# Kernel optimization log

Measured on AMD Instinct MI355X. Metric: run time of the kernel, lower is better.

The kernel has to match this reference:

```python
import jax, jax.numpy as jnp
import numpy as np

NUM_CLASSES = 10
MAX_V = 81  # max_width * max_height = 9*9


def _ln(x, w, eps=1e-5):
    # torch LayerNorm with bias=False (weight only)
    m = jnp.mean(x, axis=-1, keepdims=True)
    v = jnp.var(x, axis=-1, keepdims=True)
    return (x - m) / jnp.sqrt(v + eps) * w


def _mha(q_in, k_in, v_in, in_proj, out_proj, nhead):
    # torch nn.MultiheadAttention, bias=False
    d = q_in.shape[-1]
    Wq, Wk, Wv = in_proj[:d], in_proj[d:2 * d], in_proj[2 * d:]
    q = q_in @ Wq.T
    k = k_in @ Wk.T
    v = v_in @ Wv.T
    B, Lq, _ = q.shape
    Lk = k.shape[1]
    hd = d // nhead
    q = q.reshape(B, Lq, nhead, hd)
    k = k.reshape(B, Lk, nhead, hd)
    v = v.reshape(B, Lk, nhead, hd)
    scores = jnp.einsum('bqhd,bkhd->bhqk', q, k) / jnp.sqrt(jnp.asarray(hd, q.dtype))
    attn = jax.nn.softmax(scores, axis=-1)
    o = jnp.einsum('bhqk,bkhd->bqhd', attn, v).reshape(B, Lq, d)
    return o @ out_proj.T


def setup_inputs() -> dict:
    key = jax.random.key(0)
    ks = jax.random.split(key, 16)
    N, C, H, W = 16, NUM_CLASSES, 30, 30
    d = C + 1  # 11
    V = 32

    def rn(k, shape, s=0.2):
        return (jax.random.normal(k, shape) * s).astype(jnp.float32)

    return {
        'x': jax.random.normal(ks[0], (N, C, H, W), dtype=jnp.float32),
        'V_feature': rn(ks[1], (C, V), 1.0),
        'enc_in_proj': rn(ks[2], (3 * d, d)),
        'enc_out_proj': rn(ks[3], (d, d)),
        'enc_lin1': rn(ks[4], (1, d)),
        'enc_lin2': rn(ks[5], (d, 1)),
        'enc_ln1': jnp.ones((d,), jnp.float32),
        'enc_ln2': jnp.ones((d,), jnp.float32),
        'ffV_w': rn(ks[6], (V, MAX_V)),
        'dec_sa_in': rn(ks[7], (3 * V, V)),
        'dec_sa_out': rn(ks[8], (V, V)),
        'dec_ca_in': rn(ks[9], (3 * V, V)),
        'dec_ca_out': rn(ks[10], (V, V)),
        'dec_lin1': rn(ks[11], (1, V)),
        'dec_lin2': rn(ks[12], (V, 1)),
        'dec_ln1': jnp.ones((V,), jnp.float32),
        'dec_ln2': jnp.ones((V,), jnp.float32),
        'dec_ln3': jnp.ones((V,), jnp.float32),
        'W_d0': rn(ks[13], (8, V)),
        'W_d1': rn(ks[14], (1, 8)),
    }


def reference(x, V_feature, enc_in_proj, enc_out_proj, enc_lin1, enc_lin2,
              enc_ln1, enc_ln2, ffV_w, dec_sa_in, dec_sa_out, dec_ca_in,
              dec_ca_out, dec_lin1, dec_lin2, dec_ln1, dec_ln2, dec_ln3,
              W_d0, W_d1):
    N, C, H, W = x.shape
    # PixelVectorExtractor: pad(0) + all-ones channel padded with 1, 3x3 unfold
    xp = jnp.pad(x, ((0, 0), (0, 0), (1, 1), (1, 1)))
    ones = jnp.ones((N, 1, H + 2, W + 2), x.dtype)
    xc = jnp.concatenate([xp, ones], axis=1)  # [N, C+1, H+2, W+2]
    # row-major 3x3 patch order matches torch unfold(0,3,1).unfold(1,3,1)
    patches = jnp.stack([xc[:, :, di:di + H, dj:dj + W]
                         for di in range(3) for dj in range(3)], axis=-1)
    feat = patches.transpose(0, 2, 3, 1, 4).reshape(N * H * W, C + 1, 9)
    feat = jnp.pad(feat, ((0, 0), (0, 0), (0, MAX_V - 9)))  # [B, C+1, 81]

    # TransformerEncoder (1 layer, post-norm, nhead=1, relu FF, no dropout)
    f = feat.transpose(0, 2, 1)  # [B, 81, C+1]
    f = _ln(f + _mha(f, f, f, enc_in_proj, enc_out_proj, 1), enc_ln1)
    f = _ln(f + jax.nn.relu(f @ enc_lin1.T) @ enc_lin2.T, enc_ln2)
    f = f.transpose(0, 2, 1)  # [B, C+1, 81]

    mem = f @ ffV_w.T  # ff_V: Linear(81 -> 32, no bias) -> [B, C+1, 32]
    B, _, V = mem.shape

    # TransformerDecoder (1 layer, post-norm, nhead=32 so head_dim=1)
    y = jnp.broadcast_to(V_feature, (B, C, V))
    y = _ln(y + _mha(y, y, y, dec_sa_in, dec_sa_out, V), dec_ln1)
    y = _ln(y + _mha(y, mem, mem, dec_ca_in, dec_ca_out, V), dec_ln2)
    y = _ln(y + jax.nn.relu(y @ dec_lin1.T) @ dec_lin2.T, dec_ln3)

    # decode MLP: 32 -> 8 -> 1
    y = jax.nn.relu(y @ W_d0.T) @ W_d1.T  # [B, C, 1]
    return y.reshape(N, H, W, C).transpose(0, 3, 1, 2)
```

## Files before the change

kernel.cpp:

```cpp
#include <hip/hip_runtime.h>
#include <math.h>


__device__ __forceinline__ float gsum32(float v) {
#pragma unroll
  for (int m = 16; m > 0; m >>= 1) v += __shfl_xor(v, m, 32);
  return v;
}

__device__ __forceinline__ void wsync() {
  asm volatile("s_waitcnt lgkmcnt(0)" ::: "memory");
}

__global__ __launch_bounds__(256) void precompute_kernel(
    const float* __restrict__ Vf,
    const float* __restrict__ enc_in,
    const float* __restrict__ enc_outw,
    const float* __restrict__ ffV_w,
    const float* __restrict__ dec_sa_in,
    const float* __restrict__ dec_sa_out,
    const float* __restrict__ dec_ln1,
    const float* __restrict__ dec_ca_in,
    float* __restrict__ M_enc, float* __restrict__ WVO,
    float* __restrict__ G_k, float* __restrict__ G_v,
    float* __restrict__ y1, float* __restrict__ qca)
{
  const int tid = threadIdx.x;

  if (blockIdx.x == 0) {
    const float rs11 = 0.3015113445777636f;
    for (int idx = tid; idx < 121; idx += 256) {
      int c = idx / 11, cp = idx - c * 11;
      float sm = 0.f, sv = 0.f;
      for (int i = 0; i < 11; ++i) {
        sm += enc_in[i * 11 + c] * enc_in[(11 + i) * 11 + cp];
        sv += enc_outw[c * 11 + i] * enc_in[(22 + i) * 11 + cp];
      }
      M_enc[idx] = sm * rs11;
      WVO[idx] = sv;
    }

    __shared__ float Fsh[320];
    for (int idx = tid; idx < 288; idx += 256) {
      int t = idx >> 5, j = idx & 31;
      Fsh[idx] = ffV_w[j * 81 + t];
    }
    if (tid < 32) {
      float s = 0.f;
      for (int t = 9; t < 81; ++t) s += ffV_w[tid * 81 + t];
      Fsh[288 + tid] = s;
    }
    __syncthreads();

    for (int idx = tid; idx < 640; idx += 256) {
      int which = idx >= 320;
      int r = idx - 320 * which;
      int t = r >> 5, h = r & 31;
      const float* w = dec_ca_in + ((which ? 64 : 32) + h) * 32;
      float s = 0.f;
      for (int j = 0; j < 32; ++j) s += Fsh[t * 32 + j] * w[j];
      (which ? G_v : G_k)[r] = s;
    }
  } else {
    __shared__ float qsa[320], ksa[320], vsa[320], osa[320], zb[320];
    __shared__ float mu[16], rstd[16];

    for (int idx = tid; idx < 960; idx += 256) {
      int m = idx / 320, r = idx - m * 320;
      int t = r >> 5, h = r & 31;
      const float* w = dec_sa_in + (m * 32 + h) * 32;
      const float* yr = Vf + t * 32;
      float s = 0.f;
#pragma unroll
      for (int j = 0; j < 32; ++j) s += yr[j] * w[j];
      (m == 0 ? qsa : m == 1 ? ksa : vsa)[r] = s;
    }
    __syncthreads();

    for (int idx = tid; idx < 320; idx += 256) {
      int h = idx & 31;
      float q = qsa[idx];
      float sc[10];
      float mx = -1e30f;
#pragma unroll
      for (int s = 0; s < 10; ++s) { sc[s] = q * ksa[s * 32 + h]; mx = fmaxf(mx, sc[s]); }
      float den = 0.f, acc = 0.f;
#pragma unroll
      for (int s = 0; s < 10; ++s) {
        float e = __expf(sc[s] - mx);
        den += e;
        acc += e * vsa[s * 32 + h];
      }
      osa[idx] = acc / den;
    }
    __syncthreads();

    for (int idx = tid; idx < 320; idx += 256) {
      int t = idx >> 5, c = idx & 31;
      float s = 0.f;
#pragma unroll
      for (int h = 0; h < 32; ++h) s += osa[t * 32 + h] * dec_sa_out[c * 32 + h];
      zb[idx] = Vf[idx] + s;
    }
    __syncthreads();

    if (tid < 10) {
      float s1 = 0.f, s2 = 0.f;
      for (int c = 0; c < 32; ++c) { float z = zb[tid * 32 + c]; s1 += z; s2 += z * z; }
      float m = s1 * (1.f / 32.f);
      mu[tid] = m;
      rstd[tid] = 1.f / sqrtf(s2 * (1.f / 32.f) - m * m + 1e-5f);
    }
    __syncthreads();

    for (int idx = tid; idx < 320; idx += 256) {
      int t = idx >> 5, c = idx & 31;
      float v = (zb[idx] - mu[t]) * rstd[t] * dec_ln1[c];
      y1[idx] = v;
      zb[idx] = v;
    }
    __syncthreads();

    for (int idx = tid; idx < 320; idx += 256) {
      int t = idx >> 5, h = idx & 31;
      const float* w = dec_ca_in + h * 32;
      float s = 0.f;
#pragma unroll
      for (int j = 0; j < 32; ++j) s += zb[t * 32 + j] * w[j];
      qca[idx] = s;
    }
  }
}

#define SLICE 1376

__global__ __launch_bounds__(256) void pixel_main_kernel(
    const float* __restrict__ x,
    const float* __restrict__ M_enc, const float* __restrict__ WVO,
    const float* __restrict__ enc_lin1, const float* __restrict__ enc_lin2,
    const float* __restrict__ enc_ln1, const float* __restrict__ enc_ln2,
    const float* __restrict__ G_k, const float* __restrict__ G_v,
    const float* __restrict__ y1g, const float* __restrict__ qcag,
    const float* __restrict__ dec_ca_out,
    const float* __restrict__ dec_lin1, const float* __restrict__ dec_lin2,
    const float* __restrict__ dec_ln2v, const float* __restrict__ dec_ln3v,
    const float* __restrict__ W_d0, const float* __restrict__ W_d1,
    float* __restrict__ out)
{
  __shared__ __align__(16) float sh[4 * SLICE];
  const int wave = threadIdx.x >> 6;
  const int lane = threadIdx.x & 63;
  float* ls = sh + wave * SLICE;
  const int F9 = 0, G = 112, VO = 224, SC = 336, ZR = 432, FE = 544, KC = 656, VC = 1008;
  const int OC = 0, ZB = 320;

  const int p = blockIdx.x * 4 + wave;
  const int n = p / 900;
  const int rem = p - n * 900;
  const int pi = rem / 30, pj = rem - (rem / 30) * 30;

  for (int idx = lane; idx < 99; idx += 64) {
    int t = idx / 11, c = idx - t * 11;
    float val = 1.0f;
    if (c < 10) {
      int di = t / 3, dj = t - (t / 3) * 3;
      int ii = pi + di - 1, jj = pj + dj - 1;
      val = (ii >= 0 && ii < 30 && jj >= 0 && jj < 30)
                ? x[((n * 10 + c) * 30 + ii) * 30 + jj] : 0.0f;
    }
    ls[F9 + idx] = val;
  }
  wsync();

  for (int idx = lane; idx < 99; idx += 64) {
    int s = idx / 11, c = idx - (idx / 11) * 11;
    const float* Mr = M_enc + c * 11;
    const float* Wr = WVO + c * 11;
    float ag = 0.f, av = 0.f;
#pragma unroll
    for (int cp = 0; cp < 11; ++cp) {
      float fv = ls[F9 + s * 11 + cp];
      ag += Mr[cp] * fv;
      av += Wr[cp] * fv;
    }
    ls[G + idx] = ag;
    ls[VO + idx] = av;
  }
  wsync();

  for (int idx = lane; idx < 81; idx += 64) {
    int t = idx / 9, s = idx - (idx / 9) * 9;
    float a = 0.f;
#pragma unroll
    for (int c = 0; c < 11; ++c) a += ls[F9 + t * 11 + c] * ls[G + s * 11 + c];
    ls[SC + idx] = a;
  }
  wsync();

  if (lane < 9) {
    float e[9];
    float mx = 0.0f;
#pragma unroll
    for (int s = 0; s < 9; ++s) { e[s] = ls[SC + lane * 9 + s]; mx = fmaxf(mx, e[s]); }
    float den = 72.0f * __expf(-mx);
#pragma unroll
    for (int s = 0; s < 9; ++s) {
      e[s] = __expf(e[s] - mx);
      den += e[s];
      ls[SC + lane * 9 + s] = e[s];
    }
    ls[SC + 81 + lane] = 1.0f / den;
  }
  wsync();

  for (int idx = lane; idx < 110; idx += 64) {
    int t = idx / 11, c = idx - (idx / 11) * 11;
    float a = 0.f;
    if (t < 9) {
#pragma unroll
      for (int s = 0; s < 9; ++s) a += ls[SC + t * 9 + s] * ls[VO + s * 11 + c];
      a = a * ls[SC + 81 + t] + ls[F9 + idx];
    } else {
#pragma unroll
      for (int s = 0; s < 9; ++s) a += ls[VO + s * 11 + c];
      a *= (1.0f / 81.0f);
    }
    ls[ZR + idx] = a;
  }
  wsync();

  if (lane < 10) {
    float row[11];
#pragma unroll
    for (int c = 0; c < 11; ++c) row[c] = ls[ZR + lane * 11 + c];
    float s1 = 0.f, s2 = 0.f;
#pragma unroll
    for (int c = 0; c < 11; ++c) { s1 += row[c]; s2 += row[c] * row[c]; }
    float mu = s1 * (1.0f / 11.0f);
    float rs = 1.0f / sqrtf(s2 * (1.0f / 11.0f) - mu * mu + 1e-5f);
    float h = 0.f;
#pragma unroll
    for (int c = 0; c < 11; ++c) {
      row[c] = (row[c] - mu) * rs * enc_ln1[c];
      h += row[c] * enc_lin1[c];
    }
    h = fmaxf(h, 0.f);
    float t1 = 0.f, t2 = 0.f;
#pragma unroll
    for (int c = 0; c < 11; ++c) {
      row[c] += h * enc_lin2[c];
      t1 += row[c]; t2 += row[c] * row[c];
    }
    float mu2 = t1 * (1.0f / 11.0f);
    float rs2 = 1.0f / sqrtf(t2 * (1.0f / 11.0f) - mu2 * mu2 + 1e-5f);
#pragma unroll
    for (int c = 0; c < 11; ++c)
      ls[FE + lane * 11 + c] = (row[c] - mu2) * rs2 * enc_ln2[c];
  }
  wsync();

  {
    const int h = lane & 31, grp = lane >> 5;
    const float* Gb = grp ? G_v : G_k;
    const int dst = grp ? VC : KC;
    float gr[10];
#pragma unroll
    for (int t = 0; t < 10; ++t) gr[t] = Gb[t * 32 + h];
#pragma unroll
    for (int c = 0; c < 11; ++c) {
      float a = 0.f;
#pragma unroll
      for (int t = 0; t < 10; ++t) a += ls[FE + t * 11 + c] * gr[t];
      ls[dst + c * 32 + h] = a;
    }
  }
  wsync();

  for (int it = 0; it < 5; ++it) {
    int idx = it * 64 + lane;
    int t = idx >> 5, h = idx & 31;
    float q = qcag[t * 32 + h];
    float kreg[11];
#pragma unroll
    for (int s = 0; s < 11; ++s) kreg[s] = q * ls[KC + s * 32 + h];
    float mx = kreg[0];
#pragma unroll
    for (int s = 1; s < 11; ++s) mx = fmaxf(mx, kreg[s]);
    float den = 0.f, acc = 0.f;
#pragma unroll
    for (int s = 0; s < 11; ++s) {
      float e = __expf(kreg[s] - mx);
      den += e;
      acc += e * ls[VC + s * 32 + h];
    }
    ls[OC + idx] = acc / den;
  }
  wsync();

  for (int k = 0; k < 5; ++k) {
    int t = 2 * k + (lane >> 5);
    int c = lane & 31;
    float zacc = 0.f;
    const float4* wrow = (const float4*)(dec_ca_out + c * 32);
    const float4* orow = (const float4*)(ls + OC + t * 32);
#pragma unroll
    for (int h4 = 0; h4 < 8; ++h4) {
      float4 o4 = orow[h4];
      float4 w4 = wrow[h4];
      zacc += o4.x * w4.x + o4.y * w4.y + o4.z * w4.z + o4.w * w4.w;
    }
    float z = y1g[t * 32 + c] + zacc;
    {
      float s1 = gsum32(z), s2 = gsum32(z * z);
      float mu = s1 * (1.0f / 32.0f);
      z = (z - mu) * (1.0f / sqrtf(s2 * (1.0f / 32.0f) - mu * mu + 1e-5f)) * dec_ln2v[c];
    }
    {
      float d1 = gsum32(z * dec_lin1[c]);
      z += fmaxf(d1, 0.f) * dec_lin2[c];
    }
    {
      float s1 = gsum32(z), s2 = gsum32(z * z);
      float mu = s1 * (1.0f / 32.0f);
      z = (z - mu) * (1.0f / sqrtf(s2 * (1.0f / 32.0f) - mu * mu + 1e-5f)) * dec_ln3v[c];
    }
    ls[ZB + t * 32 + c] = z;
  }
  wsync();

  for (int idx = lane; idx < 80; idx += 64) {
    int t = idx >> 3, m = idx & 7;
    const float4* arow = (const float4*)(W_d0 + m * 32);
    const float4* zrow4 = (const float4*)(ls + ZB + t * 32);
    float d = 0.f;
#pragma unroll
    for (int q4 = 0; q4 < 8; ++q4) {
      float4 a4 = arow[q4];
      float4 z4 = zrow4[q4];
      d += a4.x * z4.x + a4.y * z4.y + a4.z * z4.z + a4.w * z4.w;
    }
    ls[OC + idx] = fmaxf(d, 0.f);
  }
  wsync();

  if (lane < 10) {
    float r = 0.f;
#pragma unroll
    for (int m = 0; m < 8; ++m) r += ls[OC + lane * 8 + m] * W_d1[m];
    out[((n * 10 + lane) * 30 + pi) * 30 + pj] = r;
  }
}

extern "C" void kernel_launch(void* const* d_in, const int* in_sizes, int n_in,
                              void* d_out, int out_size, void* d_ws, size_t ws_size,
                              hipStream_t stream) {
  (void)in_sizes; (void)n_in; (void)out_size; (void)ws_size;
  const float* x          = (const float*)d_in[0];
  const float* Vf         = (const float*)d_in[1];
  const float* enc_in     = (const float*)d_in[2];
  const float* enc_outw   = (const float*)d_in[3];
  const float* enc_lin1   = (const float*)d_in[4];
  const float* enc_lin2   = (const float*)d_in[5];
  const float* enc_ln1    = (const float*)d_in[6];
  const float* enc_ln2    = (const float*)d_in[7];
  const float* ffV_w      = (const float*)d_in[8];
  const float* dec_sa_in  = (const float*)d_in[9];
  const float* dec_sa_out = (const float*)d_in[10];
  const float* dec_ca_in  = (const float*)d_in[11];
  const float* dec_ca_out = (const float*)d_in[12];
  const float* dec_lin1   = (const float*)d_in[13];
  const float* dec_lin2   = (const float*)d_in[14];
  const float* dec_ln1    = (const float*)d_in[15];
  const float* dec_ln2    = (const float*)d_in[16];
  const float* dec_ln3    = (const float*)d_in[17];
  const float* W_d0       = (const float*)d_in[18];
  const float* W_d1       = (const float*)d_in[19];
  float* out = (float*)d_out;

  float* ws    = (float*)d_ws;
  float* M_enc = ws;
  float* WVO   = ws + 128;
  float* G_k   = ws + 256;
  float* G_v   = ws + 576;
  float* y1    = ws + 896;
  float* qca   = ws + 1216;

  hipLaunchKernelGGL(precompute_kernel, dim3(2), dim3(256), 0, stream,
                     Vf, enc_in, enc_outw, ffV_w, dec_sa_in, dec_sa_out,
                     dec_ln1, dec_ca_in, M_enc, WVO, G_k, G_v, y1, qca);

  hipLaunchKernelGGL(pixel_main_kernel, dim3(3600), dim3(256), 0, stream,
                     x, M_enc, WVO, enc_lin1, enc_lin2, enc_ln1, enc_ln2,
                     G_k, G_v, y1, qca, dec_ca_out, dec_lin1, dec_lin2,
                     dec_ln2, dec_ln3, W_d0, W_d1, out);
}
```

Baseline: 171.5 us.

## Fold decoder LayerNorm/FFN/MLP tail algebraically and pad LDS layouts for vector loads

The pixel kernel's decoder tail changes. Instead of two LayerNorms, the FFN and the 32→8 MLP done with many shuffle reductions and LDS round-trips, each lane now computes 15 partial sums that are reduced with ds_swizzle. The final outputs come from constants precomputed in the setup kernel (hc). LDS arrays are padded to stride 12 so float4 loads work, the per-wave slice shrinks, and K/V for cross-attention are kept in registers and exchanged with a shuffle. Other changes: exp2 with LOG2E folded into the weights, rcp/rsq intrinsics, and encoder matrices staged in LDS. The algebraic expansion of the variance terms may lose some precision.

```diff
diff --git a/kernel.cpp b/kernel.cpp
--- a/kernel.cpp
+++ b/kernel.cpp
@@ -2,11 +2,18 @@
 #include <math.h>
 
 
-__device__ __forceinline__ float gsum32(float v) {
-#pragma unroll
-  for (int m = 16; m > 0; m >>= 1) v += __shfl_xor(v, m, 32);
-  return v;
-}
+#define LOG2E 1.4426950408889634f
+
+#define F9o   0
+#define Go    112
+#define VOTo  224
+#define SCo   368
+#define ZRo   512
+#define FETo  640
+#define OCo   0
+#define SLICE 784
+
+#define SWZ_ADD(v, pat) ((v) + __int_as_float(__builtin_amdgcn_ds_swizzle(__float_as_int(v), (pat))))
 
 __device__ __forceinline__ void wsync() {
   asm volatile("s_waitcnt lgkmcnt(0)" ::: "memory");
@@ -21,9 +28,12 @@
     const float* __restrict__ dec_sa_out,
     const float* __restrict__ dec_ln1,
     const float* __restrict__ dec_ca_in,
+    const float* __restrict__ dec_ln2v, const float* __restrict__ dec_lin1,
+    const float* __restrict__ dec_lin2, const float* __restrict__ dec_ln3v,
+    const float* __restrict__ W_d0,
     float* __restrict__ M_enc, float* __restrict__ WVO,
     float* __restrict__ G_k, float* __restrict__ G_v,
-    float* __restrict__ y1, float* __restrict__ qca)
+    float* __restrict__ y1, float* __restrict__ qca, float* __restrict__ hc)
 {
   const int tid = threadIdx.x;
 
@@ -36,7 +46,7 @@
         sm += enc_in[i * 11 + c] * enc_in[(11 + i) * 11 + cp];
         sv += enc_outw[c * 11 + i] * enc_in[(22 + i) * 11 + cp];
       }
-      M_enc[idx] = sm * rs11;
+      M_enc[idx] = sm * rs11 * LOG2E;
       WVO[idx] = sv;
     }
 
@@ -60,6 +70,25 @@
       float s = 0.f;
       for (int j = 0; j < 32; ++j) s += Fsh[t * 32 + j] * w[j];
       (which ? G_v : G_k)[r] = s;
+    }
+
+    if (tid < 8) {
+      float u = 0.f, t2 = 0.f, v = 0.f;
+      for (int c = 0; c < 32; ++c) {
+        float w0 = W_d0[tid * 32 + c] * dec_ln3v[c];
+        u += dec_ln2v[c] * w0;
+        t2 += dec_lin2[c] * w0;
+        v += w0;
+      }
+      hc[tid] = u; hc[8 + tid] = t2; hc[16 + tid] = v;
+    } else if (tid == 8) {
+      float a = 0, b = 0, c2 = 0, d = 0, e = 0, f = 0;
+      for (int c = 0; c < 32; ++c) {
+        float w2 = dec_ln2v[c], l2 = dec_lin2[c];
+        a += w2; b += w2 * dec_lin1[c]; c2 += w2 * w2;
+        d += w2 * l2; e += l2; f += l2 * l2;
+      }
+      hc[24] = a; hc[25] = b; hc[26] = c2; hc[27] = d; hc[28] = e; hc[29] = f;
     }
   } else {
     __shared__ float qsa[320], ksa[320], vsa[320], osa[320], zb[320];
@@ -127,12 +156,10 @@
       float s = 0.f;
 #pragma unroll
       for (int j = 0; j < 32; ++j) s += zb[t * 32 + j] * w[j];
-      qca[idx] = s;
+      qca[idx] = s * LOG2E;
     }
   }
 }
-
-#define SLICE 1376
 
 __global__ __launch_bounds__(256) void pixel_main_kernel(
     const float* __restrict__ x,
@@ -142,17 +169,23 @@
     const float* __restrict__ G_k, const float* __restrict__ G_v,
     const float* __restrict__ y1g, const float* __restrict__ qcag,
     const float* __restrict__ dec_ca_out,
-    const float* __restrict__ dec_lin1, const float* __restrict__ dec_lin2,
-    const float* __restrict__ dec_ln2v, const float* __restrict__ dec_ln3v,
+    const float* __restrict__ dec_ln2v, const float* __restrict__ dec_lin1,
+    const float* __restrict__ dec_lin2, const float* __restrict__ dec_ln3v,
     const float* __restrict__ W_d0, const float* __restrict__ W_d1,
+    const float* __restrict__ hc,
     float* __restrict__ out)
 {
-  __shared__ __align__(16) float sh[4 * SLICE];
+  __shared__ __align__(16) float sh[4 * SLICE + 256];
+  float* bc = sh + 4 * SLICE;
+  for (int i = threadIdx.x; i < 121; i += 256) {
+    bc[i] = M_enc[i];
+    bc[128 + i] = WVO[i];
+  }
+  __syncthreads();
+
   const int wave = threadIdx.x >> 6;
   const int lane = threadIdx.x & 63;
   float* ls = sh + wave * SLICE;
-  const int F9 = 0, G = 112, VO = 224, SC = 336, ZR = 432, FE = 544, KC = 656, VC = 1008;
-  const int OC = 0, ZB = 320;
 
   const int p = blockIdx.x * 4 + wave;
   const int n = p / 900;
@@ -168,76 +201,84 @@
       val = (ii >= 0 && ii < 30 && jj >= 0 && jj < 30)
                 ? x[((n * 10 + c) * 30 + ii) * 30 + jj] : 0.0f;
     }
-    ls[F9 + idx] = val;
-  }
+    ls[F9o + t * 12 + c] = val;
+  }
+  if (lane < 12) ls[SCo + 108 + lane] = (lane < 9) ? (1.0f / 81.0f) : 0.0f;
   wsync();
 
   for (int idx = lane; idx < 99; idx += 64) {
     int s = idx / 11, c = idx - (idx / 11) * 11;
-    const float* Mr = M_enc + c * 11;
-    const float* Wr = WVO + c * 11;
+    const float4* fr = (const float4*)(ls + F9o + s * 12);
+    float4 f0 = fr[0], f1 = fr[1], f2 = fr[2];
+    float fv[11] = {f0.x, f0.y, f0.z, f0.w, f1.x, f1.y, f1.z, f1.w, f2.x, f2.y, f2.z};
+    const float* Mr = bc + c * 11;
+    const float* Wr = bc + 128 + c * 11;
     float ag = 0.f, av = 0.f;
 #pragma unroll
-    for (int cp = 0; cp < 11; ++cp) {
-      float fv = ls[F9 + s * 11 + cp];
-      ag += Mr[cp] * fv;
-      av += Wr[cp] * fv;
-    }
-    ls[G + idx] = ag;
-    ls[VO + idx] = av;
+    for (int cp = 0; cp < 11; ++cp) { ag += Mr[cp] * fv[cp]; av += Wr[cp] * fv[cp]; }
+    ls[Go + s * 12 + c] = ag;
+    ls[VOTo + c * 12 + s] = av;
   }
   wsync();
 
   for (int idx = lane; idx < 81; idx += 64) {
     int t = idx / 9, s = idx - (idx / 9) * 9;
-    float a = 0.f;
-#pragma unroll
-    for (int c = 0; c < 11; ++c) a += ls[F9 + t * 11 + c] * ls[G + s * 11 + c];
-    ls[SC + idx] = a;
+    const float4* fr = (const float4*)(ls + F9o + t * 12);
+    const float4* gr = (const float4*)(ls + Go + s * 12);
+    float4 f0 = fr[0], f1 = fr[1], f2 = fr[2];
+    float4 g0 = gr[0], g1 = gr[1], g2 = gr[2];
+    float a = f0.x * g0.x + f0.y * g0.y + f0.z * g0.z + f0.w * g0.w
+            + f1.x * g1.x + f1.y * g1.y + f1.z * g1.z + f1.w * g1.w
+            + f2.x * g2.x + f2.y * g2.y + f2.z * g2.z;
+    ls[SCo + t * 12 + s] = a;
   }
   wsync();
 
   if (lane < 9) {
-    float e[9];
+    const float4* sr = (const float4*)(ls + SCo + lane * 12);
+    float4 s0 = sr[0], s1 = sr[1];
+    float sc[9] = {s0.x, s0.y, s0.z, s0.w, s1.x, s1.y, s1.z, s1.w,
+                   ls[SCo + lane * 12 + 8]};
     float mx = 0.0f;
 #pragma unroll
-    for (int s = 0; s < 9; ++s) { e[s] = ls[SC + lane * 9 + s]; mx = fmaxf(mx, e[s]); }
-    float den = 72.0f * __expf(-mx);
-#pragma unroll
-    for (int s = 0; s < 9; ++s) {
-      e[s] = __expf(e[s] - mx);
-      den += e[s];
-      ls[SC + lane * 9 + s] = e[s];
-    }
-    ls[SC + 81 + lane] = 1.0f / den;
+    for (int s = 0; s < 9; ++s) mx = fmaxf(mx, sc[s]);
+    float den = 72.0f * exp2f(-mx);
+    float e[12];
+    e[9] = e[10] = e[11] = 0.f;
+#pragma unroll
+    for (int s = 0; s < 9; ++s) { e[s] = exp2f(sc[s] - mx); den += e[s]; }
+    float4* dst = (float4*)(ls + SCo + lane * 12);
+    dst[0] = make_float4(e[0], e[1], e[2], e[3]);
+    dst[1] = make_float4(e[4], e[5], e[6], e[7]);
+    dst[2] = make_float4(e[8], 0.f, 0.f, 0.f);
+    ls[SCo + 120 + lane] = __builtin_amdgcn_rcpf(den);
   }
   wsync();
 
   for (int idx = lane; idx < 110; idx += 64) {
     int t = idx / 11, c = idx - (idx / 11) * 11;
-    float a = 0.f;
-    if (t < 9) {
-#pragma unroll
-      for (int s = 0; s < 9; ++s) a += ls[SC + t * 9 + s] * ls[VO + s * 11 + c];
-      a = a * ls[SC + 81 + t] + ls[F9 + idx];
-    } else {
-#pragma unroll
-      for (int s = 0; s < 9; ++s) a += ls[VO + s * 11 + c];
-      a *= (1.0f / 81.0f);
-    }
-    ls[ZR + idx] = a;
+    const float4* wr = (const float4*)(ls + SCo + t * 12);
+    const float4* vr = (const float4*)(ls + VOTo + c * 12);
+    float4 w0 = wr[0], w1 = wr[1], w2q = wr[2];
+    float4 v0 = vr[0], v1 = vr[1], v2 = vr[2];
+    float a = w0.x * v0.x + w0.y * v0.y + w0.z * v0.z + w0.w * v0.w
+            + w1.x * v1.x + w1.y * v1.y + w1.z * v1.z + w1.w * v1.w
+            + w2q.x * v2.x;
+    if (t < 9) a = a * ls[SCo + 120 + t] + ls[F9o + t * 12 + c];
+    ls[ZRo + t * 12 + c] = a;
   }
   wsync();
 
   if (lane < 10) {
-    float row[11];
-#pragma unroll
-    for (int c = 0; c < 11; ++c) row[c] = ls[ZR + lane * 11 + c];
+    const float4* zr = (const float4*)(ls + ZRo + lane * 12);
+    float4 z0 = zr[0], z1 = zr[1], z2q = zr[2];
+    float row[11] = {z0.x, z0.y, z0.z, z0.w, z1.x, z1.y, z1.z, z1.w,
+                     z2q.x, z2q.y, z2q.z};
     float s1 = 0.f, s2 = 0.f;
 #pragma unroll
     for (int c = 0; c < 11; ++c) { s1 += row[c]; s2 += row[c] * row[c]; }
     float mu = s1 * (1.0f / 11.0f);
-    float rs = 1.0f / sqrtf(s2 * (1.0f / 11.0f) - mu * mu + 1e-5f);
+    float rs = __builtin_amdgcn_rsqf(s2 * (1.0f / 11.0f) - mu * mu + 1e-5f);
     float h = 0.f;
 #pragma unroll
     for (int c = 0; c < 11; ++c) {
@@ -252,102 +293,118 @@
       t1 += row[c]; t2 += row[c] * row[c];
     }
     float mu2 = t1 * (1.0f / 11.0f);
-    float rs2 = 1.0f / sqrtf(t2 * (1.0f / 11.0f) - mu2 * mu2 + 1e-5f);
+    float rs2 = __builtin_amdgcn_rsqf(t2 * (1.0f / 11.0f) - mu2 * mu2 + 1e-5f);
 #pragma unroll
     for (int c = 0; c < 11; ++c)
-      ls[FE + lane * 11 + c] = (row[c] - mu2) * rs2 * enc_ln2[c];
-  }
-  wsync();
-
+      ls[FETo + c * 12 + lane] = (row[c] - mu2) * rs2 * enc_ln2[c];
+  }
+  wsync();
+
+  const int hh = lane & 31, grp = lane >> 5;
+  float kv[11];
   {
-    const int h = lane & 31, grp = lane >> 5;
     const float* Gb = grp ? G_v : G_k;
-    const int dst = grp ? VC : KC;
     float gr[10];
 #pragma unroll
-    for (int t = 0; t < 10; ++t) gr[t] = Gb[t * 32 + h];
-#pragma unroll
-    for (int c = 0; c < 11; ++c) {
-      float a = 0.f;
-#pragma unroll
-      for (int t = 0; t < 10; ++t) a += ls[FE + t * 11 + c] * gr[t];
-      ls[dst + c * 32 + h] = a;
-    }
-  }
-  wsync();
-
-  for (int it = 0; it < 5; ++it) {
-    int idx = it * 64 + lane;
-    int t = idx >> 5, h = idx & 31;
-    float q = qcag[t * 32 + h];
-    float kreg[11];
-#pragma unroll
-    for (int s = 0; s < 11; ++s) kreg[s] = q * ls[KC + s * 32 + h];
-    float mx = kreg[0];
-#pragma unroll
-    for (int s = 1; s < 11; ++s) mx = fmaxf(mx, kreg[s]);
+    for (int t = 0; t < 10; ++t) gr[t] = Gb[t * 32 + hh];
+#pragma unroll
+    for (int cc = 0; cc < 11; ++cc) {
+      const float4* fr = (const float4*)(ls + FETo + cc * 12);
+      float4 a = fr[0], b4 = fr[1], c4 = fr[2];
+      float fe[10] = {a.x, a.y, a.z, a.w, b4.x, b4.y, b4.z, b4.w, c4.x, c4.y};
+      float s = 0.f;
+#pragma unroll
+      for (int t = 0; t < 10; ++t) s += fe[t] * gr[t];
+      kv[cc] = s;
+    }
+  }
+  float kk[11], vv[11];
+#pragma unroll
+  for (int cc = 0; cc < 11; ++cc) {
+    float o = __shfl_xor(kv[cc], 32);
+    kk[cc] = grp ? o : kv[cc];
+    vv[cc] = grp ? kv[cc] : o;
+  }
+
+#pragma unroll
+  for (int i = 0; i < 5; ++i) {
+    int t = grp * 5 + i;
+    float q = qcag[t * 32 + hh];
+    float sc[11];
+    float mx = q * kk[0];
+    sc[0] = mx;
+#pragma unroll
+    for (int s = 1; s < 11; ++s) { sc[s] = q * kk[s]; mx = fmaxf(mx, sc[s]); }
     float den = 0.f, acc = 0.f;
 #pragma unroll
     for (int s = 0; s < 11; ++s) {
-      float e = __expf(kreg[s] - mx);
+      float e = exp2f(sc[s] - mx);
       den += e;
-      acc += e * ls[VC + s * 32 + h];
-    }
-    ls[OC + idx] = acc / den;
-  }
-  wsync();
-
+      acc += e * vv[s];
+    }
+    ls[OCo + t * 32 + hh] = acc * __builtin_amdgcn_rcpf(den);
+  }
+  wsync();
+
+  const int c = hh;
+  float w2 = dec_ln2v[c], cl1 = dec_lin1[c], cl2 = dec_lin2[c], w3 = dec_ln3v[c];
+  float cw2l1 = w2 * cl1, cw2sq = w2 * w2, cw2l2 = w2 * cl2;
+  float am[8], Uu[8], Tt[8], Vv[8], W1r[8];
+#pragma unroll
+  for (int m = 0; m < 8; ++m) {
+    am[m] = w2 * w3 * W_d0[m * 32 + c];
+    Uu[m] = hc[m]; Tt[m] = hc[8 + m]; Vv[m] = hc[16 + m]; W1r[m] = W_d1[m];
+  }
+  const float Sw2 = hc[24], Sw2l1 = hc[25], Sw2sq = hc[26], Sw2l2 = hc[27],
+              Sl2 = hc[28], Sl2sq = hc[29];
+  const float4* wrow = (const float4*)(dec_ca_out + c * 32);
+
+#pragma unroll
   for (int k = 0; k < 5; ++k) {
-    int t = 2 * k + (lane >> 5);
-    int c = lane & 31;
-    float zacc = 0.f;
-    const float4* wrow = (const float4*)(dec_ca_out + c * 32);
-    const float4* orow = (const float4*)(ls + OC + t * 32);
+    const int t = 2 * k + grp;
+    float z = y1g[t * 32 + c];
+    const float4* orow = (const float4*)(ls + OCo + t * 32);
 #pragma unroll
     for (int h4 = 0; h4 < 8; ++h4) {
       float4 o4 = orow[h4];
       float4 w4 = wrow[h4];
-      zacc += o4.x * w4.x + o4.y * w4.y + o4.z * w4.z + o4.w * w4.w;
-    }
-    float z = y1g[t * 32 + c] + zacc;
-    {
-      float s1 = gsum32(z), s2 = gsum32(z * z);
-      float mu = s1 * (1.0f / 32.0f);
-      z = (z - mu) * (1.0f / sqrtf(s2 * (1.0f / 32.0f) - mu * mu + 1e-5f)) * dec_ln2v[c];
-    }
-    {
-      float d1 = gsum32(z * dec_lin1[c]);
-      z += fmaxf(d1, 0.f) * dec_lin2[c];
-    }
-    {
-      float s1 = gsum32(z), s2 = gsum32(z * z);
-      float mu = s1 * (1.0f / 32.0f);
-      z = (z - mu) * (1.0f / sqrtf(s2 * (1.0f / 32.0f) - mu * mu + 1e-5f)) * dec_ln3v[c];
-    }
-    ls[ZB + t * 32 + c] = z;
-  }
-  wsync();
-
-  for (int idx = lane; idx < 80; idx += 64) {
-    int t = idx >> 3, m = idx & 7;
-    const float4* arow = (const float4*)(W_d0 + m * 32);
-    const float4* zrow4 = (const float4*)(ls + ZB + t * 32);
-    float d = 0.f;
-#pragma unroll
-    for (int q4 = 0; q4 < 8; ++q4) {
-      float4 a4 = arow[q4];
-      float4 z4 = zrow4[q4];
-      d += a4.x * z4.x + a4.y * z4.y + a4.z * z4.z + a4.w * z4.w;
-    }
-    ls[OC + idx] = fmaxf(d, 0.f);
-  }
-  wsync();
-
-  if (lane < 10) {
+      z += o4.x * w4.x + o4.y * w4.y + o4.z * w4.z + o4.w * w4.w;
+    }
+    float b[15];
+    b[0] = z; b[1] = z * z; b[2] = z * w2; b[3] = z * cw2l1;
+    b[4] = z * cw2sq; b[5] = b[1] * cw2sq; b[6] = z * cw2l2;
+#pragma unroll
+    for (int m = 0; m < 8; ++m) b[7 + m] = z * am[m];
+#pragma unroll
+    for (int i_ = 0; i_ < 15; ++i_) b[i_] = SWZ_ADD(b[i_], 0x041F);
+#pragma unroll
+    for (int i_ = 0; i_ < 15; ++i_) b[i_] = SWZ_ADD(b[i_], 0x081F);
+#pragma unroll
+    for (int i_ = 0; i_ < 15; ++i_) b[i_] = SWZ_ADD(b[i_], 0x101F);
+#pragma unroll
+    for (int i_ = 0; i_ < 15; ++i_) b[i_] = SWZ_ADD(b[i_], 0x201F);
+#pragma unroll
+    for (int i_ = 0; i_ < 15; ++i_) b[i_] = SWZ_ADD(b[i_], 0x401F);
+
+    const float inv32 = 1.0f / 32.0f;
+    float mu = b[0] * inv32;
+    float rs = __builtin_amdgcn_rsqf(b[1] * inv32 - mu * mu + 1e-5f);
+    float d1 = rs * (b[3] - mu * Sw2l1);
+    float h1 = fmaxf(d1, 0.f);
+    float sz2 = rs * (b[2] - mu * Sw2);
+    float sz2sq = rs * rs * (b[5] - 2.f * mu * b[4] + mu * mu * Sw2sq);
+    float sz2l2 = rs * (b[6] - mu * Sw2l2);
+    float sz3 = sz2 + h1 * Sl2;
+    float sz3q = sz2sq + 2.f * h1 * sz2l2 + h1 * h1 * Sl2sq;
+    float mu3 = sz3 * inv32;
+    float rs3 = __builtin_amdgcn_rsqf(sz3q * inv32 - mu3 * mu3 + 1e-5f);
     float r = 0.f;
 #pragma unroll
-    for (int m = 0; m < 8; ++m) r += ls[OC + lane * 8 + m] * W_d1[m];
-    out[((n * 10 + lane) * 30 + pi) * 30 + pj] = r;
+    for (int m = 0; m < 8; ++m) {
+      float gm = rs3 * (rs * (b[7 + m] - mu * Uu[m]) + h1 * Tt[m] - mu3 * Vv[m]);
+      r += fmaxf(gm, 0.f) * W1r[m];
+    }
+    if (c == 0) out[((n * 10 + t) * 30 + pi) * 30 + pj] = r;
   }
 }
 
@@ -384,13 +441,15 @@
   float* G_v   = ws + 576;
   float* y1    = ws + 896;
   float* qca   = ws + 1216;
+  float* hcw   = ws + 1536;
 
   hipLaunchKernelGGL(precompute_kernel, dim3(2), dim3(256), 0, stream,
                      Vf, enc_in, enc_outw, ffV_w, dec_sa_in, dec_sa_out,
-                     dec_ln1, dec_ca_in, M_enc, WVO, G_k, G_v, y1, qca);
+                     dec_ln1, dec_ca_in, dec_ln2, dec_lin1, dec_lin2, dec_ln3,
+                     W_d0, M_enc, WVO, G_k, G_v, y1, qca, hcw);
 
   hipLaunchKernelGGL(pixel_main_kernel, dim3(3600), dim3(256), 0, stream,
                      x, M_enc, WVO, enc_lin1, enc_lin2, enc_ln1, enc_ln2,
-                     G_k, G_v, y1, qca, dec_ca_out, dec_lin1, dec_lin2,
-                     dec_ln2, dec_ln3, W_d0, W_d1, out);
+                     G_k, G_v, y1, qca, dec_ca_out, dec_ln2, dec_lin1,
+                     dec_lin2, dec_ln3, W_d0, W_d1, hcw, out);
 }
```

New measurement: 186.7 us. 1.09x slower.
